# Kernel optimization log

Measured on AMD Instinct MI355X. Metric: run time of the kernel, lower is better.

## Reference

```python
import jax, jax.numpy as jnp
import numpy as np

D = 1024
H = 16
DH = D // H  # 64


def setup_inputs() -> dict:
    key = jax.random.key(0)
    ks = jax.random.split(key, 7)
    B, S = 2, 2048
    X = jax.random.normal(ks[0], (B, S, D), dtype=jnp.float32)
    s = 1.0 / np.sqrt(D)
    # per-head projection weights stacked over heads: [H, D, DH]
    Wq = jax.random.normal(ks[1], (H, D, DH), dtype=jnp.float32) * s
    Wk = jax.random.normal(ks[2], (H, D, DH), dtype=jnp.float32) * s
    Wv = jax.random.normal(ks[3], (H, D, DH), dtype=jnp.float32) * s
    bq = jax.random.normal(ks[4], (H, DH), dtype=jnp.float32) * s
    bk = jax.random.normal(ks[5], (H, DH), dtype=jnp.float32) * s
    bv = jax.random.normal(ks[6], (H, DH), dtype=jnp.float32) * s
    return {"X": X, "Wq": Wq, "Wk": Wk, "Wv": Wv, "bq": bq, "bk": bk, "bv": bv}


def reference(X, Wq, Wk, Wv, bq, bk, bv):
    B, S, _ = X.shape
    scale = jnp.sqrt(jnp.float32(DH))
    # per-head QKV projections, vectorized over heads: [B, H, S, DH]
    Q = jnp.einsum('bsd,hde->bhse', X, Wq) + bq[None, :, None, :]
    K = jnp.einsum('bsd,hde->bhse', X, Wk) + bk[None, :, None, :]
    V = jnp.einsum('bsd,hde->bhse', X, Wv) + bv[None, :, None, :]
    # full dense scores (the original materializes them): [B, H, S, S]
    QK = jnp.einsum('bhqe,bhke->bhqk', Q, K) / scale
    # NOTE: faithful to source — softmax over full row FIRST, then tril mask
    # applied AFTER softmax (rows are NOT renormalized).
    sQK = jax.nn.softmax(QK, axis=-1) * jnp.tril(jnp.ones((S, S), dtype=QK.dtype))
    Z = jnp.einsum('bhqk,bhke->bhqe', sQK, V)  # [B, H, S, DH]
    # concat heads along feature dim in head order
    return Z.transpose(0, 2, 1, 3).reshape(B, S, H * DH)
```

## Files before the change

kernel.cpp:

```cpp
#include <hip/hip_runtime.h>
#include <hip/hip_bf16.h>
#include <hip/hip_fp16.h>

#define DD   1024
#define HH   16
#define DHH  64
#define SS   2048
#define BB   2

using f32x4 = __attribute__((ext_vector_type(4))) float;
using s16x8 = __attribute__((ext_vector_type(8))) short;
using s16x4 = __attribute__((ext_vector_type(4))) short;
using f16x8 = __attribute__((ext_vector_type(8))) _Float16;
using u32x4 = __attribute__((ext_vector_type(4))) unsigned;

#if __has_builtin(__builtin_amdgcn_exp2f)
#define EXP2(x) __builtin_amdgcn_exp2f(x)
#else
#define EXP2(x) exp2f(x)
#endif

static __device__ __forceinline__ short f2h(float x) {
    _Float16 h = (_Float16)x;
    return __builtin_bit_cast(short, h);
}
static __device__ __forceinline__ unsigned pk2(float a, float b) {
    auto h = __builtin_amdgcn_cvt_pkrtz(a, b);
    return __builtin_bit_cast(unsigned, h);
}

static __device__ __forceinline__ void glds16(const void* g, void* l) {
    __builtin_amdgcn_global_load_lds(
        (const __attribute__((address_space(1))) unsigned int*)g,
        (__attribute__((address_space(3))) unsigned int*)l, 16, 0, 0);
}

static __device__ __forceinline__ int swz(int row, int blk) {
    return row * 128 + (((blk) ^ (row & 7)) << 4);
}

static __device__ __forceinline__ f32x4 MFMA16(s16x8 a, s16x8 b, f32x4 c) {
    return __builtin_amdgcn_mfma_f32_16x16x32_f16(
        __builtin_bit_cast(f16x8, a), __builtin_bit_cast(f16x8, b), c, 0, 0, 0);
}

#define QSCALE 0.18033688011112042f

#define WT_OFF 0u
#define VT_OFF 6291456u
#define QH_OFF 14680064u
#define KH_OFF 23068672u

__global__ __launch_bounds__(256, 2) void wsplit_kernel(
    const float* __restrict__ Wq, const float* __restrict__ Wk, const float* __restrict__ Wv,
    short* __restrict__ WtG)
{
    const int dt = blockIdx.x;
    const int mh = blockIdx.y;
    const int mat = mh >> 4, h = mh & 15;
    const int d0 = dt * 64;
    const float* Wm = (mat == 0 ? Wq : (mat == 1 ? Wk : Wv)) + (size_t)h * DD * DHH;

    __shared__ float Ws[64][65];
    const int t = threadIdx.x;

#pragma unroll
    for (int i = 0; i < 4; i++) {
        int f = t + 256 * i;
        int row = f >> 4;
        int c4  = f & 15;
        float4 v = *(const float4*)(Wm + (size_t)(d0 + row) * DHH + c4 * 4);
        Ws[row][c4 * 4 + 0] = v.x;
        Ws[row][c4 * 4 + 1] = v.y;
        Ws[row][c4 * 4 + 2] = v.z;
        Ws[row][c4 * 4 + 3] = v.w;
    }
    __syncthreads();

    const int e = t >> 2, dq = t & 3;
    s16x8 h0, h1;
#pragma unroll
    for (int i = 0; i < 8; i++) h0[i] = f2h(Ws[dq * 16 + i][e]);
#pragma unroll
    for (int i = 0; i < 8; i++) h1[i] = f2h(Ws[dq * 16 + 8 + i][e]);
    size_t off = ((size_t)(mh * 64 + e)) * DD + d0 + dq * 16;
    *(s16x8*)(WtG + off)     = h0;
    *(s16x8*)(WtG + off + 8) = h1;
}

__global__ __launch_bounds__(256, 2) void proj_qk_kernel(
    const float* __restrict__ X,
    const short* __restrict__ WtG,
    const float* __restrict__ bq, const float* __restrict__ bk,
    short* __restrict__ QhG, short* __restrict__ KhG)
{
    const int s0 = blockIdx.x * 128;
    const int n0 = blockIdx.y * 128;
    __shared__ __align__(16) char smem[32768];
    const int WT = 0, XT = 16384;

    const int t = threadIdx.x;
    const int w = t >> 6, lane = t & 63, g = lane >> 4, ln = lane & 15;
    const int wm = w >> 1, wn = w & 1;

    f32x4 acc[4][4];
#pragma unroll
    for (int i = 0; i < 4; i++)
#pragma unroll
        for (int j = 0; j < 4; j++) acc[i][j] = (f32x4){0.f, 0.f, 0.f, 0.f};

    for (int d0 = 0; d0 < DD; d0 += 64) {
        if (d0) __syncthreads();
#pragma unroll
        for (int p = 0; p < 4; p++) {
            int idx = p * 256 + t;
            int row = idx >> 3, blk = idx & 7;
            size_t so = (size_t)(n0 + row) * DD + d0 + ((blk ^ (row & 7)) * 8);
            glds16(WtG + so, smem + WT + idx * 16);
        }
#pragma unroll
        for (int p = 0; p < 4; p++) {
            int idx = p * 256 + t;
            int row = idx >> 3, blk = idx & 7;
            const float* xp = X + (size_t)(s0 + row) * DD + d0 + blk * 8;
            float4 va = *(const float4*)xp;
            float4 vb = *(const float4*)(xp + 4);
            float v[8] = {va.x, va.y, va.z, va.w, vb.x, vb.y, vb.z, vb.w};
            s16x8 hv;
#pragma unroll
            for (int i = 0; i < 8; i++) hv[i] = f2h(v[i]);
            *(s16x8*)(smem + XT + swz(row, blk)) = hv;
        }
        __syncthreads();

        s16x8 bx[4][2];
#pragma unroll
        for (int nf = 0; nf < 4; nf++)
#pragma unroll
            for (int kst = 0; kst < 2; kst++)
                bx[nf][kst] = *(const s16x8*)(smem + XT + swz(64 * wn + nf * 16 + ln, kst * 4 + g));
#pragma unroll
        for (int mf = 0; mf < 4; mf++) {
            s16x8 aw[2];
#pragma unroll
            for (int kst = 0; kst < 2; kst++)
                aw[kst] = *(const s16x8*)(smem + WT + swz(64 * wm + mf * 16 + ln, kst * 4 + g));
#pragma unroll
            for (int kst = 0; kst < 2; kst++)
#pragma unroll
                for (int nf = 0; nf < 4; nf++)
                    acc[mf][nf] = MFMA16(aw[kst], bx[nf][kst], acc[mf][nf]);
        }
    }

    const int mat = n0 >> 10;
    const int h = ((n0 + 64 * wm) >> 6) & 15;
    const float* bptr = (mat ? bk : bq) + h * 64;
    short* OutP = mat ? KhG : QhG;
    const float scale = mat ? 1.0f : QSCALE;

#pragma unroll
    for (int nf = 0; nf < 4; nf++) {
        int sg = s0 + 64 * wn + nf * 16 + ln;
        int bidx = sg >> 11, sr = sg & (SS - 1);
        size_t rowbase = ((size_t)((bidx * HH + h) * SS + sr)) * DHH;
#pragma unroll
        for (int mf = 0; mf < 4; mf++) {
            float4 bias = *(const float4*)(bptr + mf * 16 + g * 4);
            float bb[4] = {bias.x, bias.y, bias.z, bias.w};
            s16x4 h4;
#pragma unroll
            for (int r = 0; r < 4; r++) h4[r] = f2h((acc[mf][nf][r] + bb[r]) * scale);
            *(s16x4*)(OutP + rowbase + mf * 16 + g * 4) = h4;
        }
    }
}

__global__ __launch_bounds__(256, 2) void proj_v_kernel(
    const float* __restrict__ X,
    const short* __restrict__ WtG,
    const float* __restrict__ bv,
    short* __restrict__ VtG)
{
    const int s0 = blockIdx.x * 128;
    const int n0 = blockIdx.y * 128;
    __shared__ __align__(16) char smem[32768];
    const int XTo = 0, WTo = 16384;

    const int t = threadIdx.x;
    const int w = t >> 6, lane = t & 63, g = lane >> 4, ln = lane & 15;
    const int wm = w >> 1, wn = w & 1;

    f32x4 acc[4][4];
#pragma unroll
    for (int i = 0; i < 4; i++)
#pragma unroll
        for (int j = 0; j < 4; j++) acc[i][j] = (f32x4){0.f, 0.f, 0.f, 0.f};

    for (int d0 = 0; d0 < DD; d0 += 64) {
        if (d0) __syncthreads();
#pragma unroll
        for (int p = 0; p < 4; p++) {
            int idx = p * 256 + t;
            int row = idx >> 3, blk = idx & 7;
            size_t so = (size_t)(2048 + n0 + row) * DD + d0 + ((blk ^ (row & 7)) * 8);
            glds16(WtG + so, smem + WTo + idx * 16);
        }
#pragma unroll
        for (int p = 0; p < 4; p++) {
            int idx = p * 256 + t;
            int row = idx >> 3, blk = idx & 7;
            const float* xp = X + (size_t)(s0 + row) * DD + d0 + blk * 8;
            float4 va = *(const float4*)xp;
            float4 vb = *(const float4*)(xp + 4);
            float v[8] = {va.x, va.y, va.z, va.w, vb.x, vb.y, vb.z, vb.w};
            s16x8 hv;
#pragma unroll
            for (int i = 0; i < 8; i++) hv[i] = f2h(v[i]);
            *(s16x8*)(smem + XTo + swz(row, blk)) = hv;
        }
        __syncthreads();

        s16x8 bw[4][2];
#pragma unroll
        for (int nf = 0; nf < 4; nf++)
#pragma unroll
            for (int kst = 0; kst < 2; kst++)
                bw[nf][kst] = *(const s16x8*)(smem + WTo + swz(64 * wn + nf * 16 + ln, kst * 4 + g));
#pragma unroll
        for (int mf = 0; mf < 4; mf++) {
            s16x8 ax[2];
#pragma unroll
            for (int kst = 0; kst < 2; kst++)
                ax[kst] = *(const s16x8*)(smem + XTo + swz(64 * wm + mf * 16 + ln, kst * 4 + g));
#pragma unroll
            for (int kst = 0; kst < 2; kst++)
#pragma unroll
                for (int nf = 0; nf < 4; nf++)
                    acc[mf][nf] = MFMA16(ax[kst], bw[nf][kst], acc[mf][nf]);
        }
    }

    const int h = ((n0 + 64 * wn) >> 6) & 15;
#pragma unroll
    for (int nf = 0; nf < 4; nf++) {
        int e = nf * 16 + ln;
        float bvv = bv[h * 64 + e];
#pragma unroll
        for (int mf = 0; mf < 4; mf++) {
            int sgb = s0 + 64 * wm + mf * 16 + g * 4;
            int bidx = sgb >> 11, sr = sgb & (SS - 1);
            s16x4 v4;
#pragma unroll
            for (int r = 0; r < 4; r++) v4[r] = f2h(acc[mf][nf][r] + bvv);
            size_t base = ((size_t)(bidx * HH + h)) * (SS * DHH);
            int idx = ((((((sr >> 6) * 2 + ((sr >> 5) & 1)) * 4 + nf) * 4
                        + ((sr >> 3) & 3)) * 16 + ln) << 3) + (sr & 7);
            *(s16x4*)(VtG + base + idx) = v4;
        }
    }
}

__global__ __launch_bounds__(256, 4) void attn_kernel(
    const short* __restrict__ QhG, const short* __restrict__ KhG,
    const short* __restrict__ VtG,
    float* __restrict__ out)
{
    const int wid = (blockIdx.x & 7) * 128 + (blockIdx.x >> 3);
    const int qraw = wid & 31, h = (wid >> 5) & 15, b = wid >> 9;
    const int qt = ((wid >> 5) & 1) ? (31 - qraw) : qraw;
    const int q0 = qt * 64;
    const size_t ho = (size_t)(b * HH + h) * SS * DHH;

    __shared__ __align__(16) char smem[16384];

    const int t = threadIdx.x;
    const int w = t >> 6, lane = t & 63, g = lane >> 4, ln = lane & 15;
    const int qrow = 16 * w + ln;
    const int qg = q0 + qrow;

    s16x8 qh[2];
#pragma unroll
    for (int kst = 0; kst < 2; kst++)
        qh[kst] = *(const s16x8*)(QhG + ho + (size_t)qg * DHH + kst * 32 + g * 8);

    int soffA[2], krowA[2];
#pragma unroll
    for (int p = 0; p < 2; p++) {
        int idx = p * 256 + t;
        int row = idx >> 3, blk = idx & 7;
        soffA[p] = (blk ^ (row & 7)) * 8;
        krowA[p] = ((row >> 5) & 1) * 32 + ((row >> 2) & 3) * 8
                 + ((row >> 4) & 1) * 4 + (row & 3);
    }

    auto stageK = [&](int buf, int ktile) {
        const int k0s = ktile * 64;
#pragma unroll
        for (int p = 0; p < 2; p++) {
            int idx = p * 256 + t;
            glds16(KhG + ho + (size_t)(k0s + krowA[p]) * DHH + soffA[p],
                   smem + buf * 8192 + idx * 16);
        }
    };

    stageK(0, 0);

    f32x4 o[4];
#pragma unroll
    for (int i = 0; i < 4; i++) o[i] = (f32x4){0.f, 0.f, 0.f, 0.f};
    float lpart = 0.f;

    int cur = 0;
    for (int kt = 0; kt < SS / 64; kt++) {
        const int k0 = kt * 64;
        const bool do_pv = (kt <= qt);
        __syncthreads();

        s16x8 av[4][2];
        if (do_pv) {
#pragma unroll
            for (int mf = 0; mf < 4; mf++)
#pragma unroll
                for (int kst = 0; kst < 2; kst++)
                    av[mf][kst] = *(const s16x8*)(VtG + ho +
                        ((((((size_t)kt * 2 + kst) * 4 + mf) * 4 + g) * 16 + ln) << 3));
        }
        if (kt < SS / 64 - 1) stageK(cur ^ 1, kt + 1);

        f32x4 s[4];
#pragma unroll
        for (int i = 0; i < 4; i++) s[i] = (f32x4){0.f, 0.f, 0.f, 0.f};

        const char* Kb = smem + cur * 8192;
#pragma unroll
        for (int kst = 0; kst < 2; kst++) {
            s16x8 ak[4];
#pragma unroll
            for (int mf = 0; mf < 4; mf++)
                ak[mf] = *(const s16x8*)(Kb + swz(mf * 16 + ln, kst * 4 + g));
#pragma unroll
            for (int mf = 0; mf < 4; mf++)
                s[mf] = MFMA16(ak[mf], qh[kst], s[mf]);
        }

#pragma unroll
        for (int mf = 0; mf < 4; mf++)
#pragma unroll
            for (int r = 0; r < 4; r++)
                s[mf][r] = EXP2(s[mf][r]);
        {
            float p0 = (s[0][0] + s[0][1]) + (s[0][2] + s[0][3]);
            float p1 = (s[1][0] + s[1][1]) + (s[1][2] + s[1][3]);
            float p2 = (s[2][0] + s[2][1]) + (s[2][2] + s[2][3]);
            float p3 = (s[3][0] + s[3][1]) + (s[3][2] + s[3][3]);
            lpart += (p0 + p1) + (p2 + p3);
        }

        if (do_pv) {
            const bool diag = (kt == qt);
#pragma unroll
            for (int kst = 0; kst < 2; kst++) {
                u32x4 u;
                if (diag) {
                    int kb = k0 + kst * 32 + g * 8;
                    float pa[4], pb[4];
#pragma unroll
                    for (int r = 0; r < 4; r++) {
                        pa[r] = (kb + r     > qg) ? 0.f : s[2 * kst][r];
                        pb[r] = (kb + 4 + r > qg) ? 0.f : s[2 * kst + 1][r];
                    }
                    u.x = pk2(pa[0], pa[1]); u.y = pk2(pa[2], pa[3]);
                    u.z = pk2(pb[0], pb[1]); u.w = pk2(pb[2], pb[3]);
                } else {
                    u.x = pk2(s[2 * kst][0], s[2 * kst][1]);
                    u.y = pk2(s[2 * kst][2], s[2 * kst][3]);
                    u.z = pk2(s[2 * kst + 1][0], s[2 * kst + 1][1]);
                    u.w = pk2(s[2 * kst + 1][2], s[2 * kst + 1][3]);
                }
                s16x8 bp = __builtin_bit_cast(s16x8, u);
#pragma unroll
                for (int mf = 0; mf < 4; mf++)
                    o[mf] = MFMA16(av[mf][kst], bp, o[mf]);
            }
        }
        cur ^= 1;
    }

    {
        float l = lpart;
        l += __shfl_xor(l, 16);
        l += __shfl_xor(l, 32);
        float inv = 1.0f / l;
        float* op = out + ((size_t)(b * SS + qg)) * (HH * DHH) + h * DHH;
#pragma unroll
        for (int mf = 0; mf < 4; mf++) {
            float4 vv = {o[mf][0] * inv, o[mf][1] * inv,
                         o[mf][2] * inv, o[mf][3] * inv};
            *(float4*)(op + mf * 16 + g * 4) = vv;
        }
    }
}

extern "C" void kernel_launch(void* const* d_in, const int* in_sizes, int n_in,
                              void* d_out, int out_size, void* d_ws, size_t ws_size,
                              hipStream_t stream) {
    const float* X  = (const float*)d_in[0];
    const float* Wq = (const float*)d_in[1];
    const float* Wk = (const float*)d_in[2];
    const float* Wv = (const float*)d_in[3];
    const float* bq = (const float*)d_in[4];
    const float* bk = (const float*)d_in[5];
    const float* bv = (const float*)d_in[6];
    float* out = (float*)d_out;

    char* wsb = (char*)d_ws;
    short* Wt = (short*)(wsb + WT_OFF);
    short* Vt = (short*)(wsb + VT_OFF);
    short* Qh = (short*)(wsb + QH_OFF);
    short* Kh = (short*)(wsb + KH_OFF);

    wsplit_kernel<<<dim3(16, 48), 256, 0, stream>>>(Wq, Wk, Wv, Wt);
    proj_qk_kernel<<<dim3(32, 16), 256, 0, stream>>>(X, Wt, bq, bk, Qh, Kh);
    proj_v_kernel<<<dim3(32, 8), 256, 0, stream>>>(X, Wt, bv, Vt);
    attn_kernel<<<1024, 256, 0, stream>>>(Qh, Kh, Vt, out);
}
```

Before: 106.1 us.

## Pre-convert X to fp16 once and stage K in 128-row double-buffered tiles

```diff
diff --git a/kernel.cpp b/kernel.cpp
--- a/kernel.cpp
+++ b/kernel.cpp
@@ -50,6 +50,19 @@
 #define VT_OFF 6291456u
 #define QH_OFF 14680064u
 #define KH_OFF 23068672u
+#define XH_OFF 31457280u
+
+__global__ __launch_bounds__(256) void xconv_kernel(
+    const float* __restrict__ X, short* __restrict__ XhG)
+{
+    size_t base = ((size_t)blockIdx.x * 256 + threadIdx.x) * 8;
+    float4 a = *(const float4*)(X + base);
+    float4 b = *(const float4*)(X + base + 4);
+    s16x8 hv;
+    hv[0] = f2h(a.x); hv[1] = f2h(a.y); hv[2] = f2h(a.z); hv[3] = f2h(a.w);
+    hv[4] = f2h(b.x); hv[5] = f2h(b.y); hv[6] = f2h(b.z); hv[7] = f2h(b.w);
+    *(s16x8*)(XhG + base) = hv;
+}
 
 __global__ __launch_bounds__(256, 2) void wsplit_kernel(
     const float* __restrict__ Wq, const float* __restrict__ Wk, const float* __restrict__ Wv,
@@ -89,7 +102,7 @@
 }
 
 __global__ __launch_bounds__(256, 2) void proj_qk_kernel(
-    const float* __restrict__ X,
+    const short* __restrict__ XhG,
     const short* __restrict__ WtG,
     const float* __restrict__ bq, const float* __restrict__ bk,
     short* __restrict__ QhG, short* __restrict__ KhG)
@@ -115,21 +128,9 @@
         for (int p = 0; p < 4; p++) {
             int idx = p * 256 + t;
             int row = idx >> 3, blk = idx & 7;
-            size_t so = (size_t)(n0 + row) * DD + d0 + ((blk ^ (row & 7)) * 8);
-            glds16(WtG + so, smem + WT + idx * 16);
-        }
-#pragma unroll
-        for (int p = 0; p < 4; p++) {
-            int idx = p * 256 + t;
-            int row = idx >> 3, blk = idx & 7;
-            const float* xp = X + (size_t)(s0 + row) * DD + d0 + blk * 8;
-            float4 va = *(const float4*)xp;
-            float4 vb = *(const float4*)(xp + 4);
-            float v[8] = {va.x, va.y, va.z, va.w, vb.x, vb.y, vb.z, vb.w};
-            s16x8 hv;
-#pragma unroll
-            for (int i = 0; i < 8; i++) hv[i] = f2h(v[i]);
-            *(s16x8*)(smem + XT + swz(row, blk)) = hv;
+            int soff = (blk ^ (row & 7)) * 8;
+            glds16(WtG + (size_t)(n0 + row) * DD + d0 + soff, smem + WT + idx * 16);
+            glds16(XhG + (size_t)(s0 + row) * DD + d0 + soff, smem + XT + idx * 16);
         }
         __syncthreads();
 
@@ -177,7 +178,7 @@
 }
 
 __global__ __launch_bounds__(256, 2) void proj_v_kernel(
-    const float* __restrict__ X,
+    const short* __restrict__ XhG,
     const short* __restrict__ WtG,
     const float* __restrict__ bv,
     short* __restrict__ VtG)
@@ -203,21 +204,9 @@
         for (int p = 0; p < 4; p++) {
             int idx = p * 256 + t;
             int row = idx >> 3, blk = idx & 7;
-            size_t so = (size_t)(2048 + n0 + row) * DD + d0 + ((blk ^ (row & 7)) * 8);
-            glds16(WtG + so, smem + WTo + idx * 16);
-        }
-#pragma unroll
-        for (int p = 0; p < 4; p++) {
-            int idx = p * 256 + t;
-            int row = idx >> 3, blk = idx & 7;
-            const float* xp = X + (size_t)(s0 + row) * DD + d0 + blk * 8;
-            float4 va = *(const float4*)xp;
-            float4 vb = *(const float4*)(xp + 4);
-            float v[8] = {va.x, va.y, va.z, va.w, vb.x, vb.y, vb.z, vb.w};
-            s16x8 hv;
-#pragma unroll
-            for (int i = 0; i < 8; i++) hv[i] = f2h(v[i]);
-            *(s16x8*)(smem + XTo + swz(row, blk)) = hv;
+            int soff = (blk ^ (row & 7)) * 8;
+            glds16(WtG + (size_t)(2048 + n0 + row) * DD + d0 + soff, smem + WTo + idx * 16);
+            glds16(XhG + (size_t)(s0 + row) * DD + d0 + soff, smem + XTo + idx * 16);
         }
         __syncthreads();
 
@@ -272,7 +261,7 @@
     const int q0 = qt * 64;
     const size_t ho = (size_t)(b * HH + h) * SS * DHH;
 
-    __shared__ __align__(16) char smem[16384];
+    __shared__ __align__(16) char smem[32768];
 
     const int t = threadIdx.x;
     const int w = t >> 6, lane = t & 63, g = lane >> 4, ln = lane & 15;
@@ -284,23 +273,25 @@
     for (int kst = 0; kst < 2; kst++)
         qh[kst] = *(const s16x8*)(QhG + ho + (size_t)qg * DHH + kst * 32 + g * 8);
 
-    int soffA[2], krowA[2];
-#pragma unroll
-    for (int p = 0; p < 2; p++) {
+    int soffA[4], krowA[4];
+#pragma unroll
+    for (int p = 0; p < 4; p++) {
         int idx = p * 256 + t;
         int row = idx >> 3, blk = idx & 7;
-        soffA[p] = (blk ^ (row & 7)) * 8;
-        krowA[p] = ((row >> 5) & 1) * 32 + ((row >> 2) & 3) * 8
-                 + ((row >> 4) & 1) * 4 + (row & 3);
-    }
-
-    auto stageK = [&](int buf, int ktile) {
-        const int k0s = ktile * 64;
-#pragma unroll
-        for (int p = 0; p < 2; p++) {
+        int lrow = row & 63, sub = row >> 6;
+        soffA[p] = (blk ^ (lrow & 7)) * 8;
+        krowA[p] = sub * 64
+                 + ((lrow >> 5) & 1) * 32 + ((lrow >> 2) & 3) * 8
+                 + ((lrow >> 4) & 1) * 4 + (lrow & 3);
+    }
+
+    auto stageK = [&](int buf, int it) {
+        const int k0s = it * 128;
+#pragma unroll
+        for (int p = 0; p < 4; p++) {
             int idx = p * 256 + t;
             glds16(KhG + ho + (size_t)(k0s + krowA[p]) * DHH + soffA[p],
-                   smem + buf * 8192 + idx * 16);
+                   smem + buf * 16384 + idx * 16);
         }
     };
 
@@ -312,76 +303,82 @@
     float lpart = 0.f;
 
     int cur = 0;
-    for (int kt = 0; kt < SS / 64; kt++) {
-        const int k0 = kt * 64;
-        const bool do_pv = (kt <= qt);
+    for (int it = 0; it < SS / 128; it++) {
         __syncthreads();
-
-        s16x8 av[4][2];
-        if (do_pv) {
+        if (it < SS / 128 - 1) stageK(cur ^ 1, it + 1);
+        const char* Kbase = smem + cur * 16384;
+
+#pragma unroll
+        for (int ss = 0; ss < 2; ss++) {
+            const int kt2 = it * 2 + ss;
+            const int k0 = kt2 * 64;
+            const bool do_pv = (kt2 <= qt);
+
+            s16x8 av[4][2];
+            if (do_pv) {
+#pragma unroll
+                for (int mf = 0; mf < 4; mf++)
+#pragma unroll
+                    for (int kst = 0; kst < 2; kst++)
+                        av[mf][kst] = *(const s16x8*)(VtG + ho +
+                            ((((((size_t)kt2 * 2 + kst) * 4 + mf) * 4 + g) * 16 + ln) << 3));
+            }
+
+            f32x4 s[4];
+#pragma unroll
+            for (int i = 0; i < 4; i++) s[i] = (f32x4){0.f, 0.f, 0.f, 0.f};
+
+            const char* Kb = Kbase + ss * 8192;
+#pragma unroll
+            for (int kst = 0; kst < 2; kst++) {
+                s16x8 ak[4];
+#pragma unroll
+                for (int mf = 0; mf < 4; mf++)
+                    ak[mf] = *(const s16x8*)(Kb + swz(mf * 16 + ln, kst * 4 + g));
+#pragma unroll
+                for (int mf = 0; mf < 4; mf++)
+                    s[mf] = MFMA16(ak[mf], qh[kst], s[mf]);
+            }
+
 #pragma unroll
             for (int mf = 0; mf < 4; mf++)
 #pragma unroll
-                for (int kst = 0; kst < 2; kst++)
-                    av[mf][kst] = *(const s16x8*)(VtG + ho +
-                        ((((((size_t)kt * 2 + kst) * 4 + mf) * 4 + g) * 16 + ln) << 3));
-        }
-        if (kt < SS / 64 - 1) stageK(cur ^ 1, kt + 1);
-
-        f32x4 s[4];
-#pragma unroll
-        for (int i = 0; i < 4; i++) s[i] = (f32x4){0.f, 0.f, 0.f, 0.f};
-
-        const char* Kb = smem + cur * 8192;
-#pragma unroll
-        for (int kst = 0; kst < 2; kst++) {
-            s16x8 ak[4];
-#pragma unroll
-            for (int mf = 0; mf < 4; mf++)
-                ak[mf] = *(const s16x8*)(Kb + swz(mf * 16 + ln, kst * 4 + g));
-#pragma unroll
-            for (int mf = 0; mf < 4; mf++)
-                s[mf] = MFMA16(ak[mf], qh[kst], s[mf]);
-        }
-
-#pragma unroll
-        for (int mf = 0; mf < 4; mf++)
-#pragma unroll
-            for (int r = 0; r < 4; r++)
-                s[mf][r] = EXP2(s[mf][r]);
-        {
-            float p0 = (s[0][0] + s[0][1]) + (s[0][2] + s[0][3]);
-            float p1 = (s[1][0] + s[1][1]) + (s[1][2] + s[1][3]);
-            float p2 = (s[2][0] + s[2][1]) + (s[2][2] + s[2][3]);
-            float p3 = (s[3][0] + s[3][1]) + (s[3][2] + s[3][3]);
-            lpart += (p0 + p1) + (p2 + p3);
-        }
-
-        if (do_pv) {
-            const bool diag = (kt == qt);
-#pragma unroll
-            for (int kst = 0; kst < 2; kst++) {
-                u32x4 u;
-                if (diag) {
-                    int kb = k0 + kst * 32 + g * 8;
-                    float pa[4], pb[4];
-#pragma unroll
-                    for (int r = 0; r < 4; r++) {
-                        pa[r] = (kb + r     > qg) ? 0.f : s[2 * kst][r];
-                        pb[r] = (kb + 4 + r > qg) ? 0.f : s[2 * kst + 1][r];
+                for (int r = 0; r < 4; r++)
+                    s[mf][r] = EXP2(s[mf][r]);
+            {
+                float p0 = (s[0][0] + s[0][1]) + (s[0][2] + s[0][3]);
+                float p1 = (s[1][0] + s[1][1]) + (s[1][2] + s[1][3]);
+                float p2 = (s[2][0] + s[2][1]) + (s[2][2] + s[2][3]);
+                float p3 = (s[3][0] + s[3][1]) + (s[3][2] + s[3][3]);
+                lpart += (p0 + p1) + (p2 + p3);
+            }
+
+            if (do_pv) {
+                const bool diag = (kt2 == qt);
+#pragma unroll
+                for (int kst = 0; kst < 2; kst++) {
+                    u32x4 u;
+                    if (diag) {
+                        int kb = k0 + kst * 32 + g * 8;
+                        float pa[4], pb[4];
+#pragma unroll
+                        for (int r = 0; r < 4; r++) {
+                            pa[r] = (kb + r     > qg) ? 0.f : s[2 * kst][r];
+                            pb[r] = (kb + 4 + r > qg) ? 0.f : s[2 * kst + 1][r];
+                        }
+                        u.x = pk2(pa[0], pa[1]); u.y = pk2(pa[2], pa[3]);
+                        u.z = pk2(pb[0], pb[1]); u.w = pk2(pb[2], pb[3]);
+                    } else {
+                        u.x = pk2(s[2 * kst][0], s[2 * kst][1]);
+                        u.y = pk2(s[2 * kst][2], s[2 * kst][3]);
+                        u.z = pk2(s[2 * kst + 1][0], s[2 * kst + 1][1]);
+                        u.w = pk2(s[2 * kst + 1][2], s[2 * kst + 1][3]);
                     }
-                    u.x = pk2(pa[0], pa[1]); u.y = pk2(pa[2], pa[3]);
-                    u.z = pk2(pb[0], pb[1]); u.w = pk2(pb[2], pb[3]);
-                } else {
-                    u.x = pk2(s[2 * kst][0], s[2 * kst][1]);
-                    u.y = pk2(s[2 * kst][2], s[2 * kst][3]);
-                    u.z = pk2(s[2 * kst + 1][0], s[2 * kst + 1][1]);
-                    u.w = pk2(s[2 * kst + 1][2], s[2 * kst + 1][3]);
+                    s16x8 bp = __builtin_bit_cast(s16x8, u);
+#pragma unroll
+                    for (int mf = 0; mf < 4; mf++)
+                        o[mf] = MFMA16(av[mf][kst], bp, o[mf]);
                 }
-                s16x8 bp = __builtin_bit_cast(s16x8, u);
-#pragma unroll
-                for (int mf = 0; mf < 4; mf++)
-                    o[mf] = MFMA16(av[mf][kst], bp, o[mf]);
             }
         }
         cur ^= 1;
@@ -419,9 +416,11 @@
     short* Vt = (short*)(wsb + VT_OFF);
     short* Qh = (short*)(wsb + QH_OFF);
     short* Kh = (short*)(wsb + KH_OFF);
-
+    short* Xh = (short*)(wsb + XH_OFF);
+
+    xconv_kernel<<<2048, 256, 0, stream>>>(X, Xh);
     wsplit_kernel<<<dim3(16, 48), 256, 0, stream>>>(Wq, Wk, Wv, Wt);
-    proj_qk_kernel<<<dim3(32, 16), 256, 0, stream>>>(X, Wt, bq, bk, Qh, Kh);
-    proj_v_kernel<<<dim3(32, 8), 256, 0, stream>>>(X, Wt, bv, Vt);
+    proj_qk_kernel<<<dim3(32, 16), 256, 0, stream>>>(Xh, Wt, bq, bk, Qh, Kh);
+    proj_v_kernel<<<dim3(32, 8), 256, 0, stream>>>(Xh, Wt, bv, Vt);
     attn_kernel<<<1024, 256, 0, stream>>>(Qh, Kh, Vt, out);
 }
```

Measured after the change: 122.9 us. +15.8%, slower.
